# Kernel tuning notes

Hardware: AMD Instinct MI355X
Metric: run time of the kernel (lower is better)

## Reference

```python
import jax, jax.numpy as jnp
import numpy as np


def setup_inputs() -> dict:
    key = jax.random.key(0)
    k1, k2, k3 = jax.random.split(key, 3)
    S, B, H, D = 1024, 32, 512, 1024  # max_len, batch, bin_rnn_size, bin_rep_size
    hidden = jax.random.normal(k1, (2, B, H), dtype=jnp.float32)
    encoder_outputs = jax.random.normal(k2, (S, B, D), dtype=jnp.float32)
    # nn.Linear(D, D) params; scale W for numerically sane softmax logits
    W = jax.random.normal(k3, (D, D), dtype=jnp.float32) / np.float32(np.sqrt(D))
    b = jnp.zeros((D,), dtype=jnp.float32)
    return {"hidden": hidden, "encoder_outputs": encoder_outputs, "W": W, "b": b}


def reference(hidden, encoder_outputs, W, b):
    # method == 'general'
    B = hidden.shape[1]
    # torch.reshape((-1, B, 2H)).squeeze() == C-order flatten -> [B, 2H]
    h = hidden.reshape(B, -1)                                   # [B, D]
    energy = jnp.einsum('sbd,ed->sbe', encoder_outputs, W) + b  # Linear: x @ W.T + b
    # batch_product_luong + sum over features == contraction
    attn_energies = jnp.einsum('bd,sbd->bs', h, energy)         # [B, S]
    alpha = jax.nn.softmax(attn_energies, axis=1)[:, None, :]   # [B, 1, S]
    # alpha.bmm(encoder_outputs.transpose(0,1)) -> [B, 1, D]
    reps = jnp.einsum('bos,sbd->bod', alpha, encoder_outputs)
    return (reps, alpha)
```

## Files before the change

kernel.cpp:

```cpp
#include <hip/hip_runtime.h>

#define S 1024
#define B 32
#define D 1024
#define NCH 32
#define CH (S / NCH)
#define RPW (CH / 4)
#define ECH 16
#define EC (D / ECH)

__global__ __launch_bounds__(256) void k1_gW(const float* __restrict__ hid,
                                             const float* __restrict__ W,
                                             float* __restrict__ g) {
    const int tid = threadIdx.x;
    const int d   = blockIdx.x * 256 + tid;
    const int e0  = blockIdx.y * EC;
    __shared__ float4 sh[EC * 8];
    for (int k = 0; k < (EC * 32) / 256; ++k) {
        int lin = tid + k * 256;
        int b = lin >> 6;
        int e = lin & (EC - 1);
        ((float*)sh)[e * 32 + b] = hid[b * D + e0 + e];
    }
    __syncthreads();
    float acc[32];
    #pragma unroll
    for (int b = 0; b < 32; ++b) acc[b] = 0.f;
    for (int e = 0; e < EC; ++e) {
        float w = W[(size_t)(e0 + e) * D + d];
        #pragma unroll
        for (int j = 0; j < 8; ++j) {
            float4 hv = sh[e * 8 + j];
            acc[4 * j + 0] += hv.x * w;
            acc[4 * j + 1] += hv.y * w;
            acc[4 * j + 2] += hv.z * w;
            acc[4 * j + 3] += hv.w * w;
        }
    }
    #pragma unroll
    for (int b = 0; b < 32; ++b) atomicAdd(&g[b * D + d], acc[b]);
}

__global__ __launch_bounds__(256) void k2_fused(const float* __restrict__ enc,
                                                const float* __restrict__ g,
                                                float* __restrict__ logits,
                                                float* __restrict__ marr,
                                                float* __restrict__ larr,
                                                float* __restrict__ pacc) {
    const int tid  = threadIdx.x;
    const int lane = tid & 63;
    const int wid  = tid >> 6;
    const int c    = blockIdx.x;
    const int b    = blockIdx.y;

    const float4* gp = (const float4*)(g + b * D);
    float4 gv[4];
    #pragma unroll
    for (int j = 0; j < 4; ++j) gv[j] = gp[j * 64 + lane];

    const float4* encb = (const float4*)enc;
    const int row0 = c * CH + wid * RPW;
    const size_t rstride = (size_t)B * (D / 4);
    size_t base = ((size_t)row0 * B + b) * (D / 4) + lane;

    float4 cur[4], nxt[4];
    #pragma unroll
    for (int j = 0; j < 4; ++j) cur[j] = encb[base + j * 64];

    float m = -3.0e38f, l = 0.f;
    float4 acc[4] = {{0,0,0,0},{0,0,0,0},{0,0,0,0},{0,0,0,0}};

    for (int i = 0; i < RPW; ++i) {
        if (i + 1 < RPW) {
            size_t nb = base + (size_t)(i + 1) * rstride;
            #pragma unroll
            for (int j = 0; j < 4; ++j) nxt[j] = encb[nb + j * 64];
        }
        float pd = 0.f;
        #pragma unroll
        for (int j = 0; j < 4; ++j)
            pd += cur[j].x * gv[j].x + cur[j].y * gv[j].y +
                  cur[j].z * gv[j].z + cur[j].w * gv[j].w;
        #pragma unroll
        for (int off = 1; off < 64; off <<= 1)
            pd += __shfl_xor(pd, off, 64);
        if (lane == 0) logits[b * S + row0 + i] = pd;
        float mn = fmaxf(m, pd);
        float sc = __expf(m - mn);
        float p  = __expf(pd - mn);
        l = l * sc + p;
        #pragma unroll
        for (int j = 0; j < 4; ++j) {
            acc[j].x = acc[j].x * sc + p * cur[j].x;
            acc[j].y = acc[j].y * sc + p * cur[j].y;
            acc[j].z = acc[j].z * sc + p * cur[j].z;
            acc[j].w = acc[j].w * sc + p * cur[j].w;
        }
        m = mn;
        #pragma unroll
        for (int j = 0; j < 4; ++j) cur[j] = nxt[j];
    }

    __shared__ float4 sacc[4][256];
    __shared__ float  sm[4], sl[4];
    #pragma unroll
    for (int j = 0; j < 4; ++j) sacc[wid][j * 64 + lane] = acc[j];
    if (lane == 0) { sm[wid] = m; sl[wid] = l; }
    __syncthreads();
    float mg = fmaxf(fmaxf(sm[0], sm[1]), fmaxf(sm[2], sm[3]));
    float4 r = {0, 0, 0, 0};
    float lsum = 0.f;
    #pragma unroll
    for (int w = 0; w < 4; ++w) {
        float fw = __expf(sm[w] - mg);
        float4 a = sacc[w][wid * 64 + lane];
        r.x += a.x * fw; r.y += a.y * fw; r.z += a.z * fw; r.w += a.w * fw;
        lsum += sl[w] * fw;
    }
    ((float4*)pacc)[(size_t)(c * B + b) * (D / 4) + wid * 64 + lane] = r;
    if (tid == 0) { marr[c * B + b] = mg; larr[c * B + b] = lsum; }
}

__global__ __launch_bounds__(256) void k3_combine(const float* __restrict__ logits,
                                                  const float* __restrict__ marr,
                                                  const float* __restrict__ larr,
                                                  const float* __restrict__ pacc,
                                                  float* __restrict__ out) {
    const int tid = threadIdx.x;
    const int q   = blockIdx.x;
    const int b   = blockIdx.y;
    __shared__ float shm[NCH], shl[NCH];
    if (tid < NCH) { shm[tid] = marr[tid * B + b]; shl[tid] = larr[tid * B + b]; }
    __syncthreads();
    float mg = -3.0e38f;
    #pragma unroll
    for (int c = 0; c < NCH; ++c) mg = fmaxf(mg, shm[c]);
    const int d = q * 256 + tid;
    float lg = 0.f, racc = 0.f;
    #pragma unroll 4
    for (int c = 0; c < NCH; ++c) {
        float fc = __expf(shm[c] - mg);
        lg   += shl[c] * fc;
        racc += pacc[(size_t)(c * B + b) * D + d] * fc;
    }
    float inv = 1.f / lg;
    out[b * D + d] = racc * inv;
    int s = q * 256 + tid;
    out[B * D + b * S + s] = __expf(logits[b * S + s] - mg) * inv;
}

extern "C" void kernel_launch(void* const* d_in, const int* in_sizes, int n_in,
                              void* d_out, int out_size, void* d_ws, size_t ws_size,
                              hipStream_t stream) {
    const float* hid = (const float*)d_in[0];
    const float* enc = (const float*)d_in[1];
    const float* W   = (const float*)d_in[2];

    float* out = (float*)d_out;

    float* g      = (float*)d_ws;
    float* logits = g + B * D;
    float* marr   = logits + B * S;
    float* larr   = marr + NCH * B;
    float* pacc   = larr + NCH * B;

    hipMemsetAsync(g, 0, B * D * sizeof(float), stream);
    k1_gW<<<dim3(D / 256, ECH), 256, 0, stream>>>(hid, W, g);
    k2_fused<<<dim3(NCH, B), 256, 0, stream>>>(enc, g, logits, marr, larr, pacc);
    k3_combine<<<dim3(4, B), 256, 0, stream>>>(logits, marr, larr, pacc, out);
}
```

Baseline: 51.53 us.

## Replace atomic gW and combine kernel with partial sums and last-block combine

Drops the memset and the atomicAdd-based h·W kernel. Each block now writes a partial g per e-chunk, and every kB block sums the 8 partials itself. The separate combine kernel is folded into kB: an agent-scope counter picks the last chunk block per batch, which does the softmax normalisation and writes the outputs with float4 accesses. This cuts launches from four to two and removes atomic contention. The cost is redundant partial-sum reads of g in every kB block and a fence-plus-counter sync.

Measured after the change: 190.6 us. 3.7x slower.

```diff
diff --git a/kernel.cpp b/kernel.cpp
--- a/kernel.cpp
+++ b/kernel.cpp
@@ -4,59 +4,83 @@
 #define B 32
 #define D 1024
 #define NCH 32
-#define CH (S / NCH)
-#define RPW (CH / 4)
-#define ECH 16
-#define EC (D / ECH)
+#define CH 32
+#define RPW 8
+#define ECH 8
+#define EC 128
 
-__global__ __launch_bounds__(256) void k1_gW(const float* __restrict__ hid,
-                                             const float* __restrict__ W,
-                                             float* __restrict__ g) {
+#define PG_OFF   0
+#define LOG_OFF  (PG_OFF + ECH * B * D)
+#define MARR_OFF (LOG_OFF + B * S)
+#define LARR_OFF (MARR_OFF + NCH * B)
+#define PACC_OFF (LARR_OFF + NCH * B)
+#define CNT_OFF  (PACC_OFF + NCH * B * D)
+
+__global__ __launch_bounds__(256) void kA(const float* __restrict__ hid,
+                                          const float* __restrict__ W,
+                                          float* __restrict__ ws) {
     const int tid = threadIdx.x;
-    const int d   = blockIdx.x * 256 + tid;
-    const int e0  = blockIdx.y * EC;
-    __shared__ float4 sh[EC * 8];
-    for (int k = 0; k < (EC * 32) / 256; ++k) {
+    if (blockIdx.x == 0 && tid < B) ((int*)(ws + CNT_OFF))[tid] = 0;
+
+    const int ec = blockIdx.x >> 5;
+    const int dc = blockIdx.x & 31;
+    __shared__ float h_sh[EC * 33];
+    #pragma unroll
+    for (int k = 0; k < (EC * B) / 256; ++k) {
         int lin = tid + k * 256;
-        int b = lin >> 6;
+        int b = lin >> 7;
         int e = lin & (EC - 1);
-        ((float*)sh)[e * 32 + b] = hid[b * D + e0 + e];
+        h_sh[e * 33 + b] = hid[b * D + ec * EC + e];
     }
     __syncthreads();
-    float acc[32];
-    #pragma unroll
-    for (int b = 0; b < 32; ++b) acc[b] = 0.f;
+
+    const int dq = tid & 7;
+    const int b  = tid >> 3;
+    const float4* W4 = (const float4*)W;
+    float4 a4 = {0.f, 0.f, 0.f, 0.f};
     for (int e = 0; e < EC; ++e) {
-        float w = W[(size_t)(e0 + e) * D + d];
-        #pragma unroll
-        for (int j = 0; j < 8; ++j) {
-            float4 hv = sh[e * 8 + j];
-            acc[4 * j + 0] += hv.x * w;
-            acc[4 * j + 1] += hv.y * w;
-            acc[4 * j + 2] += hv.z * w;
-            acc[4 * j + 3] += hv.w * w;
-        }
+        float h  = h_sh[e * 33 + b];
+        float4 w = W4[((size_t)(ec * EC + e) * D + dc * 32) / 4 + dq];
+        a4.x += h * w.x; a4.y += h * w.y; a4.z += h * w.z; a4.w += h * w.w;
     }
-    #pragma unroll
-    for (int b = 0; b < 32; ++b) atomicAdd(&g[b * D + d], acc[b]);
+    float* pg = ws + PG_OFF;
+    ((float4*)(pg + (size_t)(ec * B + b) * D + dc * 32))[dq] = a4;
 }
 
-__global__ __launch_bounds__(256) void k2_fused(const float* __restrict__ enc,
-                                                const float* __restrict__ g,
-                                                float* __restrict__ logits,
-                                                float* __restrict__ marr,
-                                                float* __restrict__ larr,
-                                                float* __restrict__ pacc) {
+__global__ __launch_bounds__(256) void kB(const float* __restrict__ enc,
+                                          float* __restrict__ out,
+                                          float* __restrict__ ws) {
     const int tid  = threadIdx.x;
     const int lane = tid & 63;
     const int wid  = tid >> 6;
     const int c    = blockIdx.x;
     const int b    = blockIdx.y;
 
-    const float4* gp = (const float4*)(g + b * D);
+    float* pg     = ws + PG_OFF;
+    float* logits = ws + LOG_OFF;
+    float* marr   = ws + MARR_OFF;
+    float* larr   = ws + LARR_OFF;
+    float* pacc   = ws + PACC_OFF;
+    int*   cnt    = (int*)(ws + CNT_OFF);
+
+    __shared__ float4 sacc[4 * 256];
+    __shared__ float sm[4], sl[4];
+    __shared__ int sflag;
+
+    {
+        float4 s4 = {0.f, 0.f, 0.f, 0.f};
+        #pragma unroll
+        for (int ec = 0; ec < ECH; ++ec) {
+            float4 v = ((const float4*)(pg + (size_t)(ec * B + b) * D))[tid];
+            s4.x += v.x; s4.y += v.y; s4.z += v.z; s4.w += v.w;
+        }
+        sacc[tid] = s4;
+    }
+    __syncthreads();
     float4 gv[4];
     #pragma unroll
-    for (int j = 0; j < 4; ++j) gv[j] = gp[j * 64 + lane];
+    for (int j = 0; j < 4; ++j) gv[j] = sacc[j * 64 + lane];
+    __syncthreads();
 
     const float4* encb = (const float4*)enc;
     const int row0 = c * CH + wid * RPW;
@@ -101,52 +125,58 @@
         for (int j = 0; j < 4; ++j) cur[j] = nxt[j];
     }
 
-    __shared__ float4 sacc[4][256];
-    __shared__ float  sm[4], sl[4];
     #pragma unroll
-    for (int j = 0; j < 4; ++j) sacc[wid][j * 64 + lane] = acc[j];
+    for (int j = 0; j < 4; ++j) sacc[wid * 256 + j * 64 + lane] = acc[j];
     if (lane == 0) { sm[wid] = m; sl[wid] = l; }
     __syncthreads();
-    float mg = fmaxf(fmaxf(sm[0], sm[1]), fmaxf(sm[2], sm[3]));
-    float4 r = {0, 0, 0, 0};
-    float lsum = 0.f;
-    #pragma unroll
-    for (int w = 0; w < 4; ++w) {
-        float fw = __expf(sm[w] - mg);
-        float4 a = sacc[w][wid * 64 + lane];
-        r.x += a.x * fw; r.y += a.y * fw; r.z += a.z * fw; r.w += a.w * fw;
-        lsum += sl[w] * fw;
+    {
+        float mg = fmaxf(fmaxf(sm[0], sm[1]), fmaxf(sm[2], sm[3]));
+        float4 r = {0.f, 0.f, 0.f, 0.f};
+        float lsum = 0.f;
+        #pragma unroll
+        for (int w = 0; w < 4; ++w) {
+            float fw = __expf(sm[w] - mg);
+            float4 a = sacc[w * 256 + wid * 64 + lane];
+            r.x += a.x * fw; r.y += a.y * fw; r.z += a.z * fw; r.w += a.w * fw;
+            lsum += sl[w] * fw;
+        }
+        ((float4*)pacc)[(size_t)(c * B + b) * (D / 4) + wid * 64 + lane] = r;
+        if (tid == 0) { marr[c * B + b] = mg; larr[c * B + b] = lsum; }
     }
-    ((float4*)pacc)[(size_t)(c * B + b) * (D / 4) + wid * 64 + lane] = r;
-    if (tid == 0) { marr[c * B + b] = mg; larr[c * B + b] = lsum; }
-}
 
-__global__ __launch_bounds__(256) void k3_combine(const float* __restrict__ logits,
-                                                  const float* __restrict__ marr,
-                                                  const float* __restrict__ larr,
-                                                  const float* __restrict__ pacc,
-                                                  float* __restrict__ out) {
-    const int tid = threadIdx.x;
-    const int q   = blockIdx.x;
-    const int b   = blockIdx.y;
-    __shared__ float shm[NCH], shl[NCH];
+    __threadfence();
+    if (tid == 0) {
+        int old = __hip_atomic_fetch_add(&cnt[b], 1, __ATOMIC_ACQ_REL,
+                                         __HIP_MEMORY_SCOPE_AGENT);
+        sflag = (old == NCH - 1);
+    }
+    __syncthreads();
+    if (!sflag) return;
+    __threadfence();
+
+    float* shm = (float*)sacc;
+    float* shl = shm + NCH;
     if (tid < NCH) { shm[tid] = marr[tid * B + b]; shl[tid] = larr[tid * B + b]; }
     __syncthreads();
     float mg = -3.0e38f;
     #pragma unroll
-    for (int c = 0; c < NCH; ++c) mg = fmaxf(mg, shm[c]);
-    const int d = q * 256 + tid;
-    float lg = 0.f, racc = 0.f;
+    for (int cc = 0; cc < NCH; ++cc) mg = fmaxf(mg, shm[cc]);
+    float4 racc = {0.f, 0.f, 0.f, 0.f};
+    float lg = 0.f;
     #pragma unroll 4
-    for (int c = 0; c < NCH; ++c) {
-        float fc = __expf(shm[c] - mg);
-        lg   += shl[c] * fc;
-        racc += pacc[(size_t)(c * B + b) * D + d] * fc;
+    for (int cc = 0; cc < NCH; ++cc) {
+        float fc = __expf(shm[cc] - mg);
+        lg += shl[cc] * fc;
+        float4 v = ((const float4*)pacc)[(size_t)(cc * B + b) * (D / 4) + tid];
+        racc.x += v.x * fc; racc.y += v.y * fc; racc.z += v.z * fc; racc.w += v.w * fc;
     }
     float inv = 1.f / lg;
-    out[b * D + d] = racc * inv;
-    int s = q * 256 + tid;
-    out[B * D + b * S + s] = __expf(logits[b * S + s] - mg) * inv;
+    float4 rep = {racc.x * inv, racc.y * inv, racc.z * inv, racc.w * inv};
+    ((float4*)out)[b * (D / 4) + tid] = rep;
+    float4 lo = ((const float4*)(logits + b * S))[tid];
+    float4 al = {__expf(lo.x - mg) * inv, __expf(lo.y - mg) * inv,
+                 __expf(lo.z - mg) * inv, __expf(lo.w - mg) * inv};
+    ((float4*)(out + B * D))[b * (S / 4) + tid] = al;
 }
 
 extern "C" void kernel_launch(void* const* d_in, const int* in_sizes, int n_in,
@@ -157,15 +187,8 @@
     const float* W   = (const float*)d_in[2];
 
     float* out = (float*)d_out;
+    float* ws  = (float*)d_ws;
 
-    float* g      = (float*)d_ws;
-    float* logits = g + B * D;
-    float* marr   = logits + B * S;
-    float* larr   = marr + NCH * B;
-    float* pacc   = larr + NCH * B;
-
-    hipMemsetAsync(g, 0, B * D * sizeof(float), stream);
-    k1_gW<<<dim3(D / 256, ECH), 256, 0, stream>>>(hid, W, g);
-    k2_fused<<<dim3(NCH, B), 256, 0, stream>>>(enc, g, logits, marr, larr, pacc);
-    k3_combine<<<dim3(4, B), 256, 0, stream>>>(logits, marr, larr, pacc, out);
+    kA<<<dim3(ECH * 32), 256, 0, stream>>>(hid, W, ws);
+    kB<<<dim3(NCH, B), 256, 0, stream>>>(enc, out, ws);
 }
```
